# Performance work log

Hardware: AMD Instinct MI355X
Metric: run time of the kernel (lower is better)

Reference implementation:

```python
import jax, jax.numpy as jnp
import numpy as np

NUM_EXPERTS = 8
TOP_K = 2
D_MODEL = 1024
EXPERT_CAP = 512  # dim_feedforward // num_experts = 4096 // 8
B, S = 4, 2048


def setup_inputs() -> dict:
    key = jax.random.key(0)
    ks = jax.random.split(key, 4)
    scale = 1.0 / np.sqrt(D_MODEL)
    x = jax.random.normal(ks[0], (B, S, D_MODEL), dtype=jnp.float32)
    gate_w = jax.random.normal(ks[1], (D_MODEL, NUM_EXPERTS), dtype=jnp.float32) * scale
    w1 = jax.random.normal(ks[2], (NUM_EXPERTS, D_MODEL, EXPERT_CAP), dtype=jnp.float32) * scale
    b1 = jnp.zeros((NUM_EXPERTS, EXPERT_CAP), dtype=jnp.float32)
    w2 = jax.random.normal(ks[3], (NUM_EXPERTS, EXPERT_CAP, D_MODEL), dtype=jnp.float32) * (1.0 / np.sqrt(EXPERT_CAP))
    b2 = jnp.zeros((NUM_EXPERTS, D_MODEL), dtype=jnp.float32)
    return {"x": x, "gate_w": gate_w, "w1": w1, "b1": b1, "w2": w2, "b2": b2}


def reference(x, gate_w, w1, b1, w2, b2):
    Bx, Sx, D = x.shape
    xt = x.reshape(-1, D)  # [N, D], N = B*S
    gates = jax.nn.softmax(xt @ gate_w, axis=-1)           # [N, E]
    topk_g, topk_i = jax.lax.top_k(gates, TOP_K)           # [N, K]
    # Faithful to source: every selected expert is scaled by the SUM of all top-k gates
    tok_w = topk_g.sum(axis=-1)                            # [N]
    sel = (topk_i[:, :, None] == jnp.arange(NUM_EXPERTS)[None, None, :]).any(axis=1)  # [N, E] bool
    # Dense per-expert MLP (E small), then mask-combine (scatter-add equivalent)
    h = jax.nn.gelu(jnp.einsum('nd,edh->enh', xt, w1) + b1[:, None, :], approximate=False)  # [E, N, H]
    y = jnp.einsum('enh,ehd->end', h, w2) + b2[:, None, :]  # [E, N, D]
    out = jnp.einsum('end,ne,n->nd', y, sel.astype(x.dtype), tok_w)  # [N, D]
    return out.reshape(Bx, Sx, D)
```

## Files before the change

### kernel.cpp

```cpp
#include <hip/hip_runtime.h>
#include <math.h>

#define N_TOK 8192
#define DM 1024
#define NE 8
#define HE 512
#define NPAIR 16384

#define BM 128
#define BN 128
#define BK 64

#define GSTR 1028

typedef __bf16 bf16x8 __attribute__((ext_vector_type(8)));
typedef float f32x4 __attribute__((ext_vector_type(4)));

#define GLOBAL_AS __attribute__((address_space(1)))
#define LDS_AS    __attribute__((address_space(3)))

__device__ __forceinline__ void gl_lds16(const void* g, void* lds) {
    __builtin_amdgcn_global_load_lds((const GLOBAL_AS unsigned int*)g,
                                     (LDS_AS unsigned int*)lds, 16, 0, 0);
}

__device__ __forceinline__ unsigned short f2bf(float f) {
    unsigned int u = __float_as_uint(f);
    u += 0x7fffu + ((u >> 16) & 1u);
    return (unsigned short)(u >> 16);
}

__device__ __forceinline__ float bf2f(unsigned short u) {
    return __uint_as_float(((unsigned int)u) << 16);
}

__device__ __forceinline__ float gelu_exact(float v) {
    return 0.5f * v * (1.0f + erff(v * 0.70710678118654752440f));
}

__device__ __forceinline__ double shfl_xor_dbl(double v, int m) {
    long long l = __double_as_longlong(v);
    int lo = (int)(l & 0xffffffffll);
    int hi = (int)(l >> 32);
    lo = __shfl_xor(lo, m, 64);
    hi = __shfl_xor(hi, m, 64);
    return __longlong_as_double(((long long)hi << 32) | (unsigned long long)(unsigned int)lo);
}

__global__ void transpose_cast2_kernel(const float* __restrict__ w1,
                                       const float* __restrict__ w2,
                                       unsigned short* __restrict__ w1t,
                                       unsigned short* __restrict__ w2t) {
    __shared__ float tile[64][65];
    int z = blockIdx.z;
    const float* src; unsigned short* dst; int R, C, c0, r0;
    if (z < 8) {
        src = w1 + (size_t)z * DM * HE; dst = w1t + (size_t)z * DM * HE;
        R = DM; C = HE; c0 = blockIdx.x * 64; r0 = blockIdx.y * 64;
    } else {
        int e = z - 8;
        src = w2 + (size_t)e * HE * DM; dst = w2t + (size_t)e * HE * DM;
        R = HE; C = DM; c0 = blockIdx.y * 64; r0 = blockIdx.x * 64;
    }
    int tc = threadIdx.x & 63, tg = threadIdx.x >> 6;
    #pragma unroll
    for (int i = 0; i < 16; i++) {
        int r = tg * 16 + i;
        tile[r][tc] = src[(size_t)(r0 + r) * C + (c0 + tc)];
    }
    __syncthreads();
    #pragma unroll
    for (int i = 0; i < 16; i++) {
        int r = tg * 16 + i;
        dst[(size_t)(c0 + r) * R + (r0 + tc)] = f2bf(tile[tc][r]);
    }
}

__global__ __launch_bounds__(256) void gate_cast_kernel(
        const float* __restrict__ x, const float* __restrict__ gw,
        unsigned short* __restrict__ xb,
        float* __restrict__ w_tok, int* __restrict__ e_sel) {
    __shared__ float gls[NE * GSTR];
    int tid = threadIdx.x;
    for (int v = tid; v < 2048; v += 256) {
        float4 g4 = ((const float4*)gw)[v];
        int idx = v * 4;
        int d = idx >> 3;
        int e0 = idx & 7;
        gls[(e0    ) * GSTR + d] = g4.x;
        gls[(e0 + 1) * GSTR + d] = g4.y;
        gls[(e0 + 2) * GSTR + d] = g4.z;
        gls[(e0 + 3) * GSTR + d] = g4.w;
    }
    __syncthreads();

    int n = blockIdx.x * 4 + (tid >> 6);
    int lane = tid & 63;
    const float4* xr = (const float4*)(x + (size_t)n * DM);
    ushort4* xw = (ushort4*)(xb + (size_t)n * DM);

    double s[NE];
    #pragma unroll
    for (int e = 0; e < NE; e++) s[e] = 0.0;

    #pragma unroll
    for (int i = 0; i < 4; i++) {
        float4 x4 = xr[i * 64 + lane];
        ushort4 o;
        o.x = f2bf(x4.x); o.y = f2bf(x4.y); o.z = f2bf(x4.z); o.w = f2bf(x4.w);
        xw[i * 64 + lane] = o;
        int d = (i * 64 + lane) * 4;
        #pragma unroll
        for (int e = 0; e < NE; e++) {
            float4 g4 = *(const float4*)(&gls[e * GSTR + d]);
            s[e] += (double)x4.x * (double)g4.x + (double)x4.y * (double)g4.y
                  + (double)x4.z * (double)g4.z + (double)x4.w * (double)g4.w;
        }
    }
    #pragma unroll
    for (int e = 0; e < NE; e++) {
        for (int off = 32; off > 0; off >>= 1)
            s[e] += shfl_xor_dbl(s[e], off);
    }
    if (lane == 0) {
        double m = s[0];
        for (int e = 1; e < NE; e++) if (s[e] > m) m = s[e];
        double sum = 0.0;
        for (int e = 0; e < NE; e++) sum += exp(s[e] - m);
        int i1 = 0; double v1 = s[0];
        for (int e = 1; e < NE; e++) if (s[e] > v1) { v1 = s[e]; i1 = e; }
        int i2 = -1; double v2 = -1e300;
        for (int e = 0; e < NE; e++) if (e != i1 && s[e] > v2) { v2 = s[e]; i2 = e; }
        w_tok[n] = (float)((exp(v1 - m) + exp(v2 - m)) / sum);
        e_sel[2 * n]     = i1;
        e_sel[2 * n + 1] = i2;
    }
}

__global__ __launch_bounds__(1024) void route_kernel(
        const int* __restrict__ e_sel, int* __restrict__ cnt, int* __restrict__ offs,
        int* __restrict__ pair_tok, int* __restrict__ slotmap) {
    __shared__ int wbin[16][NE];
    __shared__ int wstart[16][NE];
    __shared__ int etot[NE], eoffs[NE];
    int tid = threadIdx.x;
    int w = tid >> 6, l = tid & 63;
    if (l < NE) wbin[w][l] = 0;
    __syncthreads();

    int sel[16];
    #pragma unroll
    for (int k = 0; k < 16; k++) {
        sel[k] = e_sel[tid * 16 + k];
        atomicAdd(&wbin[w][sel[k]], 1);
    }
    __syncthreads();

    if (tid < NE) {
        int t = 0;
        for (int ww = 0; ww < 16; ww++) t += wbin[ww][tid];
        etot[tid] = t;
    }
    __syncthreads();
    if (tid == 0) {
        int a = 0;
        for (int e = 0; e < NE; e++) { eoffs[e] = a; a += etot[e]; }
    }
    __syncthreads();
    if (tid < NE) {
        cnt[tid] = etot[tid];
        offs[tid] = eoffs[tid];
        int r = eoffs[tid];
        for (int ww = 0; ww < 16; ww++) { wstart[ww][tid] = r; r += wbin[ww][tid]; }
    }
    __syncthreads();
    if (l < NE) wbin[w][l] = wstart[w][l];
    __syncthreads();

    #pragma unroll
    for (int k = 0; k < 16; k++) {
        int i = tid * 16 + k;
        int slot = atomicAdd(&wbin[w][sel[k]], 1);
        pair_tok[slot] = i >> 1;
        slotmap[i] = slot;
    }
}

__global__ __launch_bounds__(256, 2) void gemm1_kernel(
        const unsigned short* __restrict__ xb,
        const unsigned short* __restrict__ w1t,
        const float* __restrict__ b1,
        const int* __restrict__ pair_tok,
        const int* __restrict__ cnt, const int* __restrict__ offs,
        unsigned short* __restrict__ hbuf) {
    int e = blockIdx.z;
    int cn = cnt[e];
    int m0 = blockIdx.y * BM;
    if (m0 >= cn) return;
    int n0 = blockIdx.x * BN;
    int base = offs[e];

    __shared__ __align__(16) unsigned short As[2 * BM * BK];
    __shared__ __align__(16) unsigned short Bs[2 * BN * BK];

    int tid = threadIdx.x;
    int lane = tid & 63;
    int w = tid >> 6;
    int wu = __builtin_amdgcn_readfirstlane(w);
    int l3 = lane >> 3, l7 = lane & 7;
    int g = l7 ^ l3;

    const char* aptr[4];
    const char* bptr[4];
    #pragma unroll
    for (int j = 0; j < 4; j++) {
        int row = w * 32 + j * 8 + l3;
        int r = m0 + row;
        int t = pair_tok[base + (r < cn ? r : 0)];
        aptr[j] = (const char*)xb  + (size_t)t * (DM * 2) + g * 16;
        bptr[j] = (const char*)w1t + ((size_t)e * HE + n0 + row) * (DM * 2) + g * 16;
    }

    int wm = (w & 1) * 64;
    int wn = (w >> 1) * 64;
    int fr = lane & 15;
    int fq = lane >> 4;

    f32x4 acc[4][4];
    #pragma unroll
    for (int i = 0; i < 4; i++)
        #pragma unroll
        for (int j = 0; j < 4; j++)
            acc[i][j] = (f32x4){0.f, 0.f, 0.f, 0.f};

    #pragma unroll
    for (int j = 0; j < 4; j++) {
        gl_lds16(aptr[j], (char*)As + wu * 4096 + j * 1024);
        gl_lds16(bptr[j], (char*)Bs + wu * 4096 + j * 1024);
    }

    for (int it = 0; it < DM / BK; it++) {
        int p = it & 1;
        if (it + 1 < DM / BK) {
            int kb = (it + 1) * (BK * 2);
            #pragma unroll
            for (int j = 0; j < 4; j++) {
                gl_lds16(aptr[j] + kb, (char*)As + (p ^ 1) * 16384 + wu * 4096 + j * 1024);
                gl_lds16(bptr[j] + kb, (char*)Bs + (p ^ 1) * 16384 + wu * 4096 + j * 1024);
            }
            asm volatile("s_waitcnt vmcnt(8)" ::: "memory");
        } else {
            asm volatile("s_waitcnt vmcnt(0)" ::: "memory");
        }
        __builtin_amdgcn_s_barrier();
        const char* ab = (const char*)As + p * 16384;
        const char* bb = (const char*)Bs + p * 16384;
        #pragma unroll
        for (int kk2 = 0; kk2 < 2; kk2++) {
            int sw = ((kk2 * 4 + fq) ^ (fr & 7)) << 4;
            bf16x8 af[4], bfv[4];
            #pragma unroll
            for (int i = 0; i < 4; i++)
                af[i] = *(const bf16x8*)(ab + (wm + i * 16 + fr) * 128 + sw);
            #pragma unroll
            for (int j = 0; j < 4; j++)
                bfv[j] = *(const bf16x8*)(bb + (wn + j * 16 + fr) * 128 + sw);
            #pragma unroll
            for (int i = 0; i < 4; i++)
                #pragma unroll
                for (int j = 0; j < 4; j++)
                    acc[i][j] = __builtin_amdgcn_mfma_f32_16x16x32_bf16(af[i], bfv[j], acc[i][j], 0, 0, 0);
        }
        __builtin_amdgcn_s_barrier();
    }

    #pragma unroll
    for (int j = 0; j < 4; j++) {
        int nn = n0 + wn + j * 16 + fr;
        float bias = b1[e * HE + nn];
        #pragma unroll
        for (int i = 0; i < 4; i++) {
            #pragma unroll
            for (int r = 0; r < 4; r++) {
                int mm = wm + i * 16 + fq * 4 + r;
                if (m0 + mm < cn) {
                    float v = acc[i][j][r] + bias;
                    hbuf[(size_t)(base + m0 + mm) * HE + nn] = f2bf(gelu_exact(v));
                }
            }
        }
    }
}

__global__ __launch_bounds__(256, 4) void gemm2_kernel(
        const unsigned short* __restrict__ hbuf,
        const unsigned short* __restrict__ w2t,
        const float* __restrict__ b2,
        const int* __restrict__ pair_tok,
        const float* __restrict__ w_tok,
        const int* __restrict__ cnt, const int* __restrict__ offs,
        unsigned short* __restrict__ ybuf) {
    int e = blockIdx.z;
    int cn = cnt[e];
    int m0 = blockIdx.y * BM;
    if (m0 >= cn) return;
    int n0 = blockIdx.x * BN;
    int base = offs[e];

    __shared__ __align__(16) unsigned short As[BM * BK];
    __shared__ __align__(16) unsigned short Bs[BN * BK];
    __shared__ float wts[BM];

    int tid = threadIdx.x;
    if (tid < BM) {
        int r = m0 + tid;
        int rr = (r < cn ? r : cn - 1);
        wts[tid] = w_tok[pair_tok[base + rr]];
    }
    __syncthreads();

    int lane = tid & 63;
    int w = tid >> 6;
    int wu = __builtin_amdgcn_readfirstlane(w);
    int l3 = lane >> 3, l7 = lane & 7;
    int g = l7 ^ l3;

    const char* aptr[4];
    const char* bptr[4];
    #pragma unroll
    for (int j = 0; j < 4; j++) {
        int row = w * 32 + j * 8 + l3;
        int crow = (m0 + row < cn) ? row : 0;
        aptr[j] = (const char*)hbuf + (size_t)(base + m0 + crow) * (HE * 2) + g * 16;
        bptr[j] = (const char*)w2t  + ((size_t)e * DM + n0 + row) * (HE * 2) + g * 16;
    }

    int wm = (w & 1) * 64;
    int wn = (w >> 1) * 64;
    int fr = lane & 15;
    int fq = lane >> 4;

    f32x4 acc[4][4];
    #pragma unroll
    for (int i = 0; i < 4; i++)
        #pragma unroll
        for (int j = 0; j < 4; j++)
            acc[i][j] = (f32x4){0.f, 0.f, 0.f, 0.f};

    for (int k0 = 0; k0 < HE; k0 += BK) {
        int kb = k0 * 2;
        #pragma unroll
        for (int j = 0; j < 4; j++) {
            gl_lds16(aptr[j] + kb, (char*)As + wu * 4096 + j * 1024);
            gl_lds16(bptr[j] + kb, (char*)Bs + wu * 4096 + j * 1024);
        }
        __syncthreads();
        #pragma unroll
        for (int kk2 = 0; kk2 < 2; kk2++) {
            int sw = ((kk2 * 4 + fq) ^ (fr & 7)) << 4;
            bf16x8 af[4], bfv[4];
            #pragma unroll
            for (int i = 0; i < 4; i++)
                af[i] = *(const bf16x8*)((const char*)As + (wm + i * 16 + fr) * 128 + sw);
            #pragma unroll
            for (int j = 0; j < 4; j++)
                bfv[j] = *(const bf16x8*)((const char*)Bs + (wn + j * 16 + fr) * 128 + sw);
            #pragma unroll
            for (int i = 0; i < 4; i++)
                #pragma unroll
                for (int j = 0; j < 4; j++)
                    acc[i][j] = __builtin_amdgcn_mfma_f32_16x16x32_bf16(af[i], bfv[j], acc[i][j], 0, 0, 0);
        }
        __syncthreads();
    }

    #pragma unroll
    for (int j = 0; j < 4; j++) {
        int dd = n0 + wn + j * 16 + fr;
        float bias = b2[e * DM + dd];
        #pragma unroll
        for (int i = 0; i < 4; i++) {
            #pragma unroll
            for (int r = 0; r < 4; r++) {
                int mm = wm + i * 16 + fq * 4 + r;
                if (m0 + mm < cn) {
                    float wgt = wts[mm];
                    ybuf[(size_t)(base + m0 + mm) * DM + dd] = f2bf(wgt * (acc[i][j][r] + bias));
                }
            }
        }
    }
}

__global__ void combine_kernel(const unsigned short* __restrict__ yb,
                               const int* __restrict__ slotmap,
                               float* __restrict__ out) {
    int i = blockIdx.x * 256 + threadIdx.x;
    int n = i >> 8;
    int c = (i & 255) * 4;
    int s1 = slotmap[2 * n];
    int s2 = slotmap[2 * n + 1];
    ushort4 a = *(const ushort4*)(&yb[(size_t)s1 * DM + c]);
    ushort4 b = *(const ushort4*)(&yb[(size_t)s2 * DM + c]);
    float4 o;
    o.x = bf2f(a.x) + bf2f(b.x);
    o.y = bf2f(a.y) + bf2f(b.y);
    o.z = bf2f(a.z) + bf2f(b.z);
    o.w = bf2f(a.w) + bf2f(b.w);
    ((float4*)out)[i] = o;
}

extern "C" void kernel_launch(void* const* d_in, const int* in_sizes, int n_in,
                              void* d_out, int out_size, void* d_ws, size_t ws_size,
                              hipStream_t stream) {
    const float* x  = (const float*)d_in[0];
    const float* gw = (const float*)d_in[1];
    const float* w1 = (const float*)d_in[2];
    const float* b1 = (const float*)d_in[3];
    const float* w2 = (const float*)d_in[4];
    const float* b2 = (const float*)d_in[5];
    float* out = (float*)d_out;

    char* ws = (char*)d_ws;
    unsigned short* ybuf = (unsigned short*)(ws);
    unsigned short* xb   = (unsigned short*)(ws);
    unsigned short* w1t  = (unsigned short*)(ws + 16777216);
    unsigned short* w2t  = (unsigned short*)(ws + 33554432);
    unsigned short* hbuf = (unsigned short*)(ws + 41943040);
    float* w_tok         = (float*)(ws + 58720256);
    int*   e_sel         = (int*)(ws + 58753024);
    int*   slotmap       = (int*)(ws + 58818560);
    int*   cnt           = (int*)(ws + 58884096);
    int*   offs          = (int*)(ws + 58884128);
    int*   pair_tok      = (int*)(ws + 58884224);

    transpose_cast2_kernel<<<dim3(8, 16, 16), 256, 0, stream>>>(w1, w2, w1t, w2t);
    gate_cast_kernel<<<N_TOK / 4, 256, 0, stream>>>(x, gw, xb, w_tok, e_sel);
    route_kernel<<<1, 1024, 0, stream>>>(e_sel, cnt, offs, pair_tok, slotmap);
    gemm1_kernel<<<dim3(HE / BN, N_TOK / BM, NE), 256, 0, stream>>>(
        xb, w1t, b1, pair_tok, cnt, offs, hbuf);
    gemm2_kernel<<<dim3(DM / BN, N_TOK / BM, NE), 256, 0, stream>>>(
        hbuf, w2t, b2, pair_tok, w_tok, cnt, offs, ybuf);
    combine_kernel<<<(N_TOK * DM / 4) / 256, 256, 0, stream>>>(ybuf, slotmap, out);
}
```

Before: 260.0 us.

## Compact grouped-GEMM grid with per-expert M-block table and smaller row tiles

The route kernel now builds a table that maps each compact M-block to its expert and base slot. Both expert GEMMs launch over that flattened list instead of a (M-tile, expert) grid where most blocks exit early. BM is halved to 64, giving finer granularity, less padding waste and higher occupancy (launch bounds raised to 4 blocks). In exchange, gemm1 loses its double-buffered LDS prefetch and now does a synchronous load-then-compute loop, and per-block B-tile reuse drops.

```diff
diff --git a/kernel.cpp b/kernel.cpp
--- a/kernel.cpp
+++ b/kernel.cpp
@@ -6,8 +6,9 @@
 #define NE 8
 #define HE 512
 #define NPAIR 16384
-
-#define BM 128
+#define MAXMB 264
+
+#define BM 64
 #define BN 128
 #define BK 64
 
@@ -139,10 +140,11 @@
 
 __global__ __launch_bounds__(1024) void route_kernel(
         const int* __restrict__ e_sel, int* __restrict__ cnt, int* __restrict__ offs,
-        int* __restrict__ pair_tok, int* __restrict__ slotmap) {
+        int* __restrict__ pair_tok, int* __restrict__ slotmap,
+        int* __restrict__ mb_e, int* __restrict__ mb_base, int* __restrict__ n_mb) {
     __shared__ int wbin[16][NE];
     __shared__ int wstart[16][NE];
-    __shared__ int etot[NE], eoffs[NE];
+    __shared__ int etot[NE], eoffs[NE], bofs[NE];
     int tid = threadIdx.x;
     int w = tid >> 6, l = tid & 63;
     if (l < NE) wbin[w][l] = 0;
@@ -163,8 +165,12 @@
     }
     __syncthreads();
     if (tid == 0) {
-        int a = 0;
-        for (int e = 0; e < NE; e++) { eoffs[e] = a; a += etot[e]; }
+        int a = 0, b = 0;
+        for (int e = 0; e < NE; e++) {
+            eoffs[e] = a; a += etot[e];
+            bofs[e] = b;  b += (etot[e] + BM - 1) / BM;
+        }
+        n_mb[0] = b;
     }
     __syncthreads();
     if (tid < NE) {
@@ -172,6 +178,12 @@
         offs[tid] = eoffs[tid];
         int r = eoffs[tid];
         for (int ww = 0; ww < 16; ww++) { wstart[ww][tid] = r; r += wbin[ww][tid]; }
+        int nb = (etot[tid] + BM - 1) / BM;
+        int b0 = bofs[tid];
+        for (int b = 0; b < nb; b++) {
+            mb_e[b0 + b] = tid;
+            mb_base[b0 + b] = eoffs[tid] + b * BM;
+        }
     }
     __syncthreads();
     if (l < NE) wbin[w][l] = wstart[w][l];
@@ -186,22 +198,24 @@
     }
 }
 
-__global__ __launch_bounds__(256, 2) void gemm1_kernel(
+__global__ __launch_bounds__(256, 4) void gemm1_kernel(
         const unsigned short* __restrict__ xb,
         const unsigned short* __restrict__ w1t,
         const float* __restrict__ b1,
         const int* __restrict__ pair_tok,
         const int* __restrict__ cnt, const int* __restrict__ offs,
+        const int* __restrict__ mb_e, const int* __restrict__ mb_base,
+        const int* __restrict__ n_mb,
         unsigned short* __restrict__ hbuf) {
-    int e = blockIdx.z;
-    int cn = cnt[e];
-    int m0 = blockIdx.y * BM;
-    if (m0 >= cn) return;
+    int mb = blockIdx.y;
+    if (mb >= n_mb[0]) return;
+    int e = mb_e[mb];
+    int sbase = mb_base[mb];
+    int vlim = offs[e] + cnt[e];
     int n0 = blockIdx.x * BN;
-    int base = offs[e];
-
-    __shared__ __align__(16) unsigned short As[2 * BM * BK];
-    __shared__ __align__(16) unsigned short Bs[2 * BN * BK];
+
+    __shared__ __align__(16) unsigned short As[BM * BK];
+    __shared__ __align__(16) unsigned short Bs[BN * BK];
 
     int tid = threadIdx.x;
     int lane = tid & 63;
@@ -210,68 +224,59 @@
     int l3 = lane >> 3, l7 = lane & 7;
     int g = l7 ^ l3;
 
-    const char* aptr[4];
+    const char* aptr[2];
     const char* bptr[4];
+    #pragma unroll
+    for (int j = 0; j < 2; j++) {
+        int row = w * 16 + j * 8 + l3;
+        int slot = sbase + row;
+        int t = pair_tok[slot < vlim ? slot : vlim - 1];
+        aptr[j] = (const char*)xb + (size_t)t * (DM * 2) + g * 16;
+    }
     #pragma unroll
     for (int j = 0; j < 4; j++) {
         int row = w * 32 + j * 8 + l3;
-        int r = m0 + row;
-        int t = pair_tok[base + (r < cn ? r : 0)];
-        aptr[j] = (const char*)xb  + (size_t)t * (DM * 2) + g * 16;
         bptr[j] = (const char*)w1t + ((size_t)e * HE + n0 + row) * (DM * 2) + g * 16;
     }
 
-    int wm = (w & 1) * 64;
+    int wm = (w & 1) * 32;
     int wn = (w >> 1) * 64;
     int fr = lane & 15;
     int fq = lane >> 4;
 
-    f32x4 acc[4][4];
-    #pragma unroll
-    for (int i = 0; i < 4; i++)
+    f32x4 acc[2][4];
+    #pragma unroll
+    for (int i = 0; i < 2; i++)
         #pragma unroll
         for (int j = 0; j < 4; j++)
             acc[i][j] = (f32x4){0.f, 0.f, 0.f, 0.f};
 
-    #pragma unroll
-    for (int j = 0; j < 4; j++) {
-        gl_lds16(aptr[j], (char*)As + wu * 4096 + j * 1024);
-        gl_lds16(bptr[j], (char*)Bs + wu * 4096 + j * 1024);
-    }
-
-    for (int it = 0; it < DM / BK; it++) {
-        int p = it & 1;
-        if (it + 1 < DM / BK) {
-            int kb = (it + 1) * (BK * 2);
-            #pragma unroll
-            for (int j = 0; j < 4; j++) {
-                gl_lds16(aptr[j] + kb, (char*)As + (p ^ 1) * 16384 + wu * 4096 + j * 1024);
-                gl_lds16(bptr[j] + kb, (char*)Bs + (p ^ 1) * 16384 + wu * 4096 + j * 1024);
-            }
-            asm volatile("s_waitcnt vmcnt(8)" ::: "memory");
-        } else {
-            asm volatile("s_waitcnt vmcnt(0)" ::: "memory");
-        }
-        __builtin_amdgcn_s_barrier();
-        const char* ab = (const char*)As + p * 16384;
-        const char* bb = (const char*)Bs + p * 16384;
+    for (int k0 = 0; k0 < DM; k0 += BK) {
+        int kb = k0 * 2;
+        #pragma unroll
+        for (int j = 0; j < 2; j++)
+            gl_lds16(aptr[j] + kb, (char*)As + wu * 2048 + j * 1024);
+        #pragma unroll
+        for (int j = 0; j < 4; j++)
+            gl_lds16(bptr[j] + kb, (char*)Bs + wu * 4096 + j * 1024);
+        __syncthreads();
         #pragma unroll
         for (int kk2 = 0; kk2 < 2; kk2++) {
             int sw = ((kk2 * 4 + fq) ^ (fr & 7)) << 4;
-            bf16x8 af[4], bfv[4];
-            #pragma unroll
-            for (int i = 0; i < 4; i++)
-                af[i] = *(const bf16x8*)(ab + (wm + i * 16 + fr) * 128 + sw);
+            bf16x8 af[2], bfv[4];
+            #pragma unroll
+            for (int i = 0; i < 2; i++)
+                af[i] = *(const bf16x8*)((const char*)As + (wm + i * 16 + fr) * 128 + sw);
             #pragma unroll
             for (int j = 0; j < 4; j++)
-                bfv[j] = *(const bf16x8*)(bb + (wn + j * 16 + fr) * 128 + sw);
-            #pragma unroll
-            for (int i = 0; i < 4; i++)
+                bfv[j] = *(const bf16x8*)((const char*)Bs + (wn + j * 16 + fr) * 128 + sw);
+            #pragma unroll
+            for (int i = 0; i < 2; i++)
                 #pragma unroll
                 for (int j = 0; j < 4; j++)
                     acc[i][j] = __builtin_amdgcn_mfma_f32_16x16x32_bf16(af[i], bfv[j], acc[i][j], 0, 0, 0);
         }
-        __builtin_amdgcn_s_barrier();
+        __syncthreads();
     }
 
     #pragma unroll
@@ -279,13 +284,13 @@
         int nn = n0 + wn + j * 16 + fr;
         float bias = b1[e * HE + nn];
         #pragma unroll
-        for (int i = 0; i < 4; i++) {
+        for (int i = 0; i < 2; i++) {
             #pragma unroll
             for (int r = 0; r < 4; r++) {
                 int mm = wm + i * 16 + fq * 4 + r;
-                if (m0 + mm < cn) {
+                if (sbase + mm < vlim) {
                     float v = acc[i][j][r] + bias;
-                    hbuf[(size_t)(base + m0 + mm) * HE + nn] = f2bf(gelu_exact(v));
+                    hbuf[(size_t)(sbase + mm) * HE + nn] = f2bf(gelu_exact(v));
                 }
             }
         }
@@ -299,13 +304,15 @@
         const int* __restrict__ pair_tok,
         const float* __restrict__ w_tok,
         const int* __restrict__ cnt, const int* __restrict__ offs,
+        const int* __restrict__ mb_e, const int* __restrict__ mb_base,
+        const int* __restrict__ n_mb,
         unsigned short* __restrict__ ybuf) {
-    int e = blockIdx.z;
-    int cn = cnt[e];
-    int m0 = blockIdx.y * BM;
-    if (m0 >= cn) return;
+    int mb = blockIdx.y;
+    if (mb >= n_mb[0]) return;
+    int e = mb_e[mb];
+    int sbase = mb_base[mb];
+    int vlim = offs[e] + cnt[e];
     int n0 = blockIdx.x * BN;
-    int base = offs[e];
 
     __shared__ __align__(16) unsigned short As[BM * BK];
     __shared__ __align__(16) unsigned short Bs[BN * BK];
@@ -313,9 +320,8 @@
 
     int tid = threadIdx.x;
     if (tid < BM) {
-        int r = m0 + tid;
-        int rr = (r < cn ? r : cn - 1);
-        wts[tid] = w_tok[pair_tok[base + rr]];
+        int slot = sbase + tid;
+        wts[tid] = w_tok[pair_tok[slot < vlim ? slot : vlim - 1]];
     }
     __syncthreads();
 
@@ -325,24 +331,29 @@
     int l3 = lane >> 3, l7 = lane & 7;
     int g = l7 ^ l3;
 
-    const char* aptr[4];
+    const char* aptr[2];
     const char* bptr[4];
+    #pragma unroll
+    for (int j = 0; j < 2; j++) {
+        int row = w * 16 + j * 8 + l3;
+        int slot = sbase + row;
+        int cs = (slot < vlim) ? slot : vlim - 1;
+        aptr[j] = (const char*)hbuf + (size_t)cs * (HE * 2) + g * 16;
+    }
     #pragma unroll
     for (int j = 0; j < 4; j++) {
         int row = w * 32 + j * 8 + l3;
-        int crow = (m0 + row < cn) ? row : 0;
-        aptr[j] = (const char*)hbuf + (size_t)(base + m0 + crow) * (HE * 2) + g * 16;
-        bptr[j] = (const char*)w2t  + ((size_t)e * DM + n0 + row) * (HE * 2) + g * 16;
-    }
-
-    int wm = (w & 1) * 64;
+        bptr[j] = (const char*)w2t + ((size_t)e * DM + n0 + row) * (HE * 2) + g * 16;
+    }
+
+    int wm = (w & 1) * 32;
     int wn = (w >> 1) * 64;
     int fr = lane & 15;
     int fq = lane >> 4;
 
-    f32x4 acc[4][4];
-    #pragma unroll
-    for (int i = 0; i < 4; i++)
+    f32x4 acc[2][4];
+    #pragma unroll
+    for (int i = 0; i < 2; i++)
         #pragma unroll
         for (int j = 0; j < 4; j++)
             acc[i][j] = (f32x4){0.f, 0.f, 0.f, 0.f};
@@ -350,23 +361,24 @@
     for (int k0 = 0; k0 < HE; k0 += BK) {
         int kb = k0 * 2;
         #pragma unroll
-        for (int j = 0; j < 4; j++) {
-            gl_lds16(aptr[j] + kb, (char*)As + wu * 4096 + j * 1024);
+        for (int j = 0; j < 2; j++)
+            gl_lds16(aptr[j] + kb, (char*)As + wu * 2048 + j * 1024);
+        #pragma unroll
+        for (int j = 0; j < 4; j++)
             gl_lds16(bptr[j] + kb, (char*)Bs + wu * 4096 + j * 1024);
-        }
         __syncthreads();
         #pragma unroll
         for (int kk2 = 0; kk2 < 2; kk2++) {
             int sw = ((kk2 * 4 + fq) ^ (fr & 7)) << 4;
-            bf16x8 af[4], bfv[4];
-            #pragma unroll
-            for (int i = 0; i < 4; i++)
+            bf16x8 af[2], bfv[4];
+            #pragma unroll
+            for (int i = 0; i < 2; i++)
                 af[i] = *(const bf16x8*)((const char*)As + (wm + i * 16 + fr) * 128 + sw);
             #pragma unroll
             for (int j = 0; j < 4; j++)
                 bfv[j] = *(const bf16x8*)((const char*)Bs + (wn + j * 16 + fr) * 128 + sw);
             #pragma unroll
-            for (int i = 0; i < 4; i++)
+            for (int i = 0; i < 2; i++)
                 #pragma unroll
                 for (int j = 0; j < 4; j++)
                     acc[i][j] = __builtin_amdgcn_mfma_f32_16x16x32_bf16(af[i], bfv[j], acc[i][j], 0, 0, 0);
@@ -379,13 +391,13 @@
         int dd = n0 + wn + j * 16 + fr;
         float bias = b2[e * DM + dd];
         #pragma unroll
-        for (int i = 0; i < 4; i++) {
+        for (int i = 0; i < 2; i++) {
             #pragma unroll
             for (int r = 0; r < 4; r++) {
                 int mm = wm + i * 16 + fq * 4 + r;
-                if (m0 + mm < cn) {
+                if (sbase + mm < vlim) {
                     float wgt = wts[mm];
-                    ybuf[(size_t)(base + m0 + mm) * DM + dd] = f2bf(wgt * (acc[i][j][r] + bias));
+                    ybuf[(size_t)(sbase + mm) * DM + dd] = f2bf(wgt * (acc[i][j][r] + bias));
                 }
             }
         }
@@ -433,13 +445,17 @@
     int*   cnt           = (int*)(ws + 58884096);
     int*   offs          = (int*)(ws + 58884128);
     int*   pair_tok      = (int*)(ws + 58884224);
+    int*   mb_e          = (int*)(ws + 58949760);
+    int*   mb_base       = (int*)(ws + 58950848);
+    int*   n_mb          = (int*)(ws + 58951936);
 
     transpose_cast2_kernel<<<dim3(8, 16, 16), 256, 0, stream>>>(w1, w2, w1t, w2t);
     gate_cast_kernel<<<N_TOK / 4, 256, 0, stream>>>(x, gw, xb, w_tok, e_sel);
-    route_kernel<<<1, 1024, 0, stream>>>(e_sel, cnt, offs, pair_tok, slotmap);
-    gemm1_kernel<<<dim3(HE / BN, N_TOK / BM, NE), 256, 0, stream>>>(
-        xb, w1t, b1, pair_tok, cnt, offs, hbuf);
-    gemm2_kernel<<<dim3(DM / BN, N_TOK / BM, NE), 256, 0, stream>>>(
-        hbuf, w2t, b2, pair_tok, w_tok, cnt, offs, ybuf);
+    route_kernel<<<1, 1024, 0, stream>>>(e_sel, cnt, offs, pair_tok, slotmap,
+                                         mb_e, mb_base, n_mb);
+    gemm1_kernel<<<dim3(HE / BN, MAXMB), 256, 0, stream>>>(
+        xb, w1t, b1, pair_tok, cnt, offs, mb_e, mb_base, n_mb, hbuf);
+    gemm2_kernel<<<dim3(DM / BN, MAXMB), 256, 0, stream>>>(
+        hbuf, w2t, b2, pair_tok, w_tok, cnt, offs, mb_e, mb_base, n_mb, ybuf);
     combine_kernel<<<(N_TOK * DM / 4) / 256, 256, 0, stream>>>(ybuf, slotmap, out);
 }
```

After: 235.3 us. 1.1x faster.
